# Performance work log

Hardware: AMD Instinct MI355X
Metric: run time of the kernel (lower is better)

The kernel has to match this reference:

```python
import jax, jax.numpy as jnp
import numpy as np

R = 16  # number of attention heads


def setup_inputs() -> dict:
    key = jax.random.key(0)
    ks = jax.random.split(key, 6)
    B, T, D = 2, 2048, 1024
    s = 1.0 / np.sqrt(D)
    return {
        "q": jax.random.normal(ks[0], (B, T, D), jnp.float32),
        "k": jax.random.normal(ks[1], (B, T, D), jnp.float32),
        "q_map": jax.random.normal(ks[2], (D, D), jnp.float32) * s,
        "k_map": jax.random.normal(ks[3], (D, D), jnp.float32) * s,
        "v_map": jax.random.normal(ks[4], (D, D), jnp.float32) * s,
        "output_map": jax.random.normal(ks[5], (D, D), jnp.float32) * s,
    }


def _split_heads(x, r):
    # [B, T, D] -> [B, r, T, D//r]
    B, T, D = x.shape
    return x.reshape(B, T, r, D // r).transpose(0, 2, 1, 3)


def reference(q, k, q_map, k_map, v_map, output_map):
    # v = k (the layer reuses Keys as Values)
    B, Tq, D = q.shape
    dh = D // R
    qh = _split_heads(q @ q_map, R)  # [B, r, Tq, dh]
    kh = _split_heads(k @ k_map, R)  # [B, r, Tk, dh]
    vh = _split_heads(k @ v_map, R)  # [B, r, Tk, dh]
    scale = 1.0 / jnp.sqrt(jnp.asarray(dh, qh.dtype))
    scores = jnp.einsum('brqd,brkd->brqk', qh, kh) * scale
    weights = jax.nn.softmax(scores, axis=-1)  # dropout=0 / inference -> identity
    out = jnp.einsum('brqk,brkd->brqd', weights, vh)  # [B, r, Tq, dh]
    merged = out.transpose(0, 2, 1, 3).reshape(B, Tq, D)
    return merged @ output_map
```

## Files before the change

kernel.cpp:

```cpp
#include <hip/hip_runtime.h>
#include <hip/hip_bf16.h>


typedef unsigned short u16;
typedef __attribute__((ext_vector_type(8))) short short8;
typedef __attribute__((ext_vector_type(4))) float f32x4;

__device__ __forceinline__ u16 f2bf(float f) {
  __hip_bfloat16 h = __float2bfloat16(f);
  return reinterpret_cast<u16&>(h);
}

__device__ __forceinline__ void gl_lds16(const u16* g, u16* l) {
  __builtin_amdgcn_global_load_lds(
      (const __attribute__((address_space(1))) void*)g,
      (__attribute__((address_space(3))) void*)l, 16, 0, 0);
}

template <int ROWS>
__device__ __forceinline__ void stage_tile(const u16* __restrict__ g, int gs,
                                           u16* lds, int wave, int lane) {
  const int lr8 = lane >> 3;
  const int gc = ((lane & 7) ^ lr8) * 8;
#pragma unroll
  for (int w = 0; w < ROWS / 32; ++w) {
    int t = w * 4 + wave;
    gl_lds16(g + (size_t)(t * 8 + lr8) * gs + gc, lds + t * 512);
  }
}

__global__ __launch_bounds__(256)
void convert_qk(const float4* __restrict__ q, const float4* __restrict__ k,
                u16* __restrict__ qb, u16* __restrict__ kb) {
  int i = blockIdx.x * 256 + threadIdx.x;
  float4 qv = q[i], kv = k[i];
  ushort4 qo, ko;
  qo.x = f2bf(qv.x); qo.y = f2bf(qv.y); qo.z = f2bf(qv.z); qo.w = f2bf(qv.w);
  ko.x = f2bf(kv.x); ko.y = f2bf(kv.y); ko.z = f2bf(kv.z); ko.w = f2bf(kv.w);
  reinterpret_cast<ushort4*>(qb)[i] = qo;
  reinterpret_cast<ushort4*>(kb)[i] = ko;
}

__global__ __launch_bounds__(256)
void convert_maps(const float* __restrict__ qm, const float* __restrict__ km,
                  const float* __restrict__ vm, const float* __restrict__ om,
                  u16* __restrict__ qmT, u16* __restrict__ kmT,
                  u16* __restrict__ vmT, u16* __restrict__ omT) {
  __shared__ float t[32][33];
  const float* src; u16* dst; float scale = 1.0f;
  switch (blockIdx.z) {
    case 0:  src = qm; dst = qmT; scale = 0.125f; break;
    case 1:  src = km; dst = kmT; break;
    case 2:  src = vm; dst = vmT; break;
    default: src = om; dst = omT; break;
  }
  int nb0 = blockIdx.x * 32, kb0 = blockIdx.y * 32;
  int c = threadIdx.x & 31, rq = threadIdx.x >> 5;
#pragma unroll
  for (int j = 0; j < 4; ++j)
    t[rq * 4 + j][c] = src[(size_t)(kb0 + rq * 4 + j) * 1024 + nb0 + c];
  __syncthreads();
#pragma unroll
  for (int j = 0; j < 4; ++j) {
    int nn = rq * 4 + j;
    dst[(size_t)(nb0 + nn) * 1024 + kb0 + c] = f2bf(t[c][nn] * scale);
  }
}

template <int BN, int MODE>
__global__ __launch_bounds__(256)
void gemm128(const u16* __restrict__ A, const u16* __restrict__ Bt,
             void* __restrict__ Cv, u16* __restrict__ Vt, int K, int ldc) {
  constexpr int JF = BN / 32;
  __shared__ u16 As[2][128 * 64];
  __shared__ u16 Bs[2][BN * 64];
  const int tid = threadIdx.x;
  const int wave = tid >> 6, lane = tid & 63;
  const int lr = lane & 15, lg = lane >> 4;
  const int m0 = blockIdx.y * 128, n0 = blockIdx.x * BN;
  const int wm = (wave >> 1) * 64, wn = (wave & 1) * (BN / 2);

  f32x4 acc[4][JF] = {};
  const int kT = K >> 6;
  const u16* Ab = A + (size_t)m0 * K;
  const u16* Bb = Bt + (size_t)n0 * K;

  stage_tile<128>(Ab, K, &As[0][0], wave, lane);
  stage_tile<BN>(Bb, K, &Bs[0][0], wave, lane);
  __syncthreads();

  int cur = 0;
  for (int kt = 0; kt < kT; ++kt) {
    if (kt + 1 < kT) {
      stage_tile<128>(Ab + (kt + 1) * 64, K, &As[cur ^ 1][0], wave, lane);
      stage_tile<BN>(Bb + (kt + 1) * 64, K, &Bs[cur ^ 1][0], wave, lane);
    }
#pragma unroll
    for (int ks = 0; ks < 2; ++ks) {
      short8 af[4], bfr[JF];
#pragma unroll
      for (int i = 0; i < 4; ++i) {
        int ar = wm + i * 16 + lr;
        int ac = (ks * 4 + lg) ^ (ar & 7);
        af[i] = *reinterpret_cast<const short8*>(&As[cur][ar * 64 + ac * 8]);
      }
#pragma unroll
      for (int j = 0; j < JF; ++j) {
        int br = wn + j * 16 + lr;
        int bc = (ks * 4 + lg) ^ (br & 7);
        bfr[j] = *reinterpret_cast<const short8*>(&Bs[cur][br * 64 + bc * 8]);
      }
#pragma unroll
      for (int i = 0; i < 4; ++i)
#pragma unroll
        for (int j = 0; j < JF; ++j)
          acc[i][j] = __builtin_amdgcn_mfma_f32_16x16x32_bf16(af[i], bfr[j], acc[i][j], 0, 0, 0);
    }
    __syncthreads();
    cur ^= 1;
  }

#pragma unroll
  for (int i = 0; i < 4; ++i) {
    int row0 = m0 + wm + i * 16 + lg * 4;
#pragma unroll
    for (int j = 0; j < JF; ++j) {
      int col = n0 + wn + j * 16 + lr;
      if (MODE == 2) {
#pragma unroll
        for (int r = 0; r < 4; ++r)
          ((float*)Cv)[(size_t)(row0 + r) * ldc + col] = acc[i][j][r];
      } else if (MODE == 0) {
#pragma unroll
        for (int r = 0; r < 4; ++r)
          ((u16*)Cv)[(size_t)(row0 + r) * ldc + col] = f2bf(acc[i][j][r]);
      } else {
        if (n0 < 1024) {
#pragma unroll
          for (int r = 0; r < 4; ++r)
            ((u16*)Cv)[(size_t)(row0 + r) * ldc + col] = f2bf(acc[i][j][r]);
        } else {
          int bb = row0 >> 11, kk = row0 & 2047;
          int hd = col - 1024;
          uint2 pk;
          pk.x = (unsigned)f2bf(acc[i][j][0]) | ((unsigned)f2bf(acc[i][j][1]) << 16);
          pk.y = (unsigned)f2bf(acc[i][j][2]) | ((unsigned)f2bf(acc[i][j][3]) << 16);
          *reinterpret_cast<uint2*>(&Vt[(size_t)(bb * 1024 + hd) * 2048 + kk]) = pk;
        }
      }
    }
  }
}

__global__ __launch_bounds__(256)
void attention(const u16* __restrict__ Qp, const u16* __restrict__ Kp,
               const u16* __restrict__ Vt, u16* __restrict__ merged) {
  __shared__ u16 Ks[2][64 * 64];
  __shared__ u16 Vs[2][64 * 64];
  __shared__ u16 Ps[128 * 64];
  const int tid = threadIdx.x;
  const int wave = tid >> 6, lane = tid & 63;
  const int lr = lane & 15, lg = lane >> 4;
  const int qt = blockIdx.x, h = blockIdx.y, b = blockIdx.z;
  const int q0 = qt * 128;

  short8 qf[2][2];
#pragma unroll
  for (int qm = 0; qm < 2; ++qm) {
    const size_t qrow = (size_t)(b * 2048 + q0 + wave * 32 + qm * 16 + lr);
#pragma unroll
    for (int ks = 0; ks < 2; ++ks)
      qf[qm][ks] = *reinterpret_cast<const short8*>(
          &Qp[qrow * 1024 + h * 64 + ks * 32 + lg * 8]);
  }

  f32x4 oacc[2][4] = {};
  float ell[2] = {0.f, 0.f};

  const u16* Kg = Kp + (size_t)(b * 2048) * 1024 + h * 64;
  const u16* Vg = Vt + (size_t)(b * 1024 + h * 64) * 2048;

  stage_tile<64>(Kg, 1024, &Ks[0][0], wave, lane);
  stage_tile<64>(Vg, 2048, &Vs[0][0], wave, lane);
  __syncthreads();

  int cur = 0;
  for (int ktile = 0; ktile < 32; ++ktile) {
    if (ktile + 1 < 32) {
      const int kn = (ktile + 1) * 64;
      stage_tile<64>(Kg + (size_t)kn * 1024, 1024, &Ks[cur ^ 1][0], wave, lane);
      stage_tile<64>(Vg + kn, 2048, &Vs[cur ^ 1][0], wave, lane);
    }
#pragma unroll
    for (int qm = 0; qm < 2; ++qm) {
      const int qq = wave * 32 + qm * 16 + lr;
#pragma unroll
      for (int kf = 0; kf < 4; ++kf) {
        f32x4 z = {};
#pragma unroll
        for (int ks = 0; ks < 2; ++ks) {
          int br = kf * 16 + lr;
          int bc = (ks * 4 + lg) ^ (br & 7);
          short8 kbf = *reinterpret_cast<const short8*>(&Ks[cur][br * 64 + bc * 8]);
          z = __builtin_amdgcn_mfma_f32_16x16x32_bf16(kbf, qf[qm][ks], z, 0, 0, 0);
        }
        float p0 = __expf(z[0]), p1 = __expf(z[1]);
        float p2 = __expf(z[2]), p3 = __expf(z[3]);
        ell[qm] += (p0 + p1) + (p2 + p3);
        uint2 pk;
        pk.x = (unsigned)f2bf(p0) | ((unsigned)f2bf(p1) << 16);
        pk.y = (unsigned)f2bf(p2) | ((unsigned)f2bf(p3) << 16);
        int ch = (2 * kf + (lg >> 1)) ^ (qq & 7);
        *reinterpret_cast<uint2*>(&Ps[qq * 64 + ch * 8 + (lg & 1) * 4]) = pk;
      }
    }
    asm volatile("s_waitcnt lgkmcnt(0)" ::: "memory");
    __builtin_amdgcn_sched_barrier(0);
#pragma unroll
    for (int qm = 0; qm < 2; ++qm) {
#pragma unroll
      for (int ks = 0; ks < 2; ++ks) {
        int par = wave * 32 + qm * 16 + lr;
        int pac = (ks * 4 + lg) ^ (par & 7);
        short8 pa = *reinterpret_cast<const short8*>(&Ps[par * 64 + pac * 8]);
#pragma unroll
        for (int df = 0; df < 4; ++df) {
          int vr = df * 16 + lr;
          int vc = (ks * 4 + lg) ^ (vr & 7);
          short8 vb = *reinterpret_cast<const short8*>(&Vs[cur][vr * 64 + vc * 8]);
          oacc[qm][df] = __builtin_amdgcn_mfma_f32_16x16x32_bf16(pa, vb, oacc[qm][df], 0, 0, 0);
        }
      }
    }
    __syncthreads();
    cur ^= 1;
  }
#pragma unroll
  for (int qm = 0; qm < 2; ++qm) {
    float e = ell[qm];
    e += __shfl_xor(e, 16);
    e += __shfl_xor(e, 32);
    float inv = 1.0f / e;
    float invr[4];
#pragma unroll
    for (int r = 0; r < 4; ++r) invr[r] = __shfl(inv, lg * 4 + r);
    const size_t rowbase = (size_t)(b * 2048 + q0 + wave * 32 + qm * 16 + lg * 4);
#pragma unroll
    for (int df = 0; df < 4; ++df)
#pragma unroll
      for (int r = 0; r < 4; ++r)
        merged[(rowbase + r) * 1024 + h * 64 + df * 16 + lr] =
            f2bf(oacc[qm][df][r] * invr[r]);
  }
}

extern "C" void kernel_launch(void* const* d_in, const int* in_sizes, int n_in,
                              void* d_out, int out_size, void* d_ws, size_t ws_size,
                              hipStream_t stream) {
  const float* q  = (const float*)d_in[0];
  const float* k  = (const float*)d_in[1];
  const float* qm = (const float*)d_in[2];
  const float* km = (const float*)d_in[3];
  const float* vm = (const float*)d_in[4];
  const float* om = (const float*)d_in[5];
  float* out = (float*)d_out;

  char* w = (char*)d_ws;
  const size_t MB = 1024 * 1024;
  u16* qb  = (u16*)(w + 0 * MB);
  u16* kb  = (u16*)(w + 8 * MB);
  u16* qmT = (u16*)(w + 16 * MB);
  u16* kmT = (u16*)(w + 18 * MB);
  u16* vmT = (u16*)(w + 20 * MB);
  u16* omT = (u16*)(w + 22 * MB);
  u16* Qp  = (u16*)(w + 24 * MB);
  u16* Kp  = (u16*)(w + 32 * MB);
  u16* Vt  = (u16*)(w + 48 * MB);
  u16* merged = qb;

  convert_qk<<<4096, 256, 0, stream>>>((const float4*)q, (const float4*)k, qb, kb);
  convert_maps<<<dim3(32, 32, 4), 256, 0, stream>>>(qm, km, vm, om, qmT, kmT, vmT, omT);
  gemm128<64, 0><<<dim3(16, 32), 256, 0, stream>>>(qb, qmT, Qp, nullptr, 1024, 1024);
  gemm128<128, 1><<<dim3(16, 32), 256, 0, stream>>>(kb, kmT, Kp, Vt, 1024, 1024);
  attention<<<dim3(16, 16, 2), 256, 0, stream>>>(Qp, Kp, Vt, merged);
  gemm128<64, 2><<<dim3(16, 32), 256, 0, stream>>>(merged, omT, out, nullptr, 1024, 1024);
}
```

Measured before the change: 219.1 us.

## Merge QKV projection GEMMs and pass attention probabilities through registers

The Q projection and the K/V projection become one launch, gemm_qkv, which treats the contiguous transposed Q, K and V maps as one 3072-column B matrix and picks the A input and output layout from the block column. The attention kernel now gives each wave a single 16-row query fragment, so blocks hold 64 queries and the grid doubles. Softmax probabilities move from the score-MFMA output layout into the PV-MFMA operand layout with cross-lane shuffles instead of a round trip through shared memory. This removes a kernel launch, the P shared-memory buffer and its wait, and should raise occupancy. The cost is extra shuffle instructions, and K/V tiles are now reloaded for half as many queries per block.

Measured after the change: 242.9 us. +10.9%, slower.

```diff
diff --git a/kernel.cpp b/kernel.cpp
--- a/kernel.cpp
+++ b/kernel.cpp
@@ -67,37 +67,115 @@
   }
 }
 
-template <int BN, int MODE>
-__global__ __launch_bounds__(256)
-void gemm128(const u16* __restrict__ A, const u16* __restrict__ Bt,
-             void* __restrict__ Cv, u16* __restrict__ Vt, int K, int ldc) {
-  constexpr int JF = BN / 32;
+__global__ __launch_bounds__(256)
+void gemm_qkv(const u16* __restrict__ qb, const u16* __restrict__ kb,
+              const u16* __restrict__ Bt, u16* __restrict__ Qp,
+              u16* __restrict__ Kp, u16* __restrict__ Vt) {
   __shared__ u16 As[2][128 * 64];
-  __shared__ u16 Bs[2][BN * 64];
+  __shared__ u16 Bs[2][128 * 64];
   const int tid = threadIdx.x;
   const int wave = tid >> 6, lane = tid & 63;
   const int lr = lane & 15, lg = lane >> 4;
-  const int m0 = blockIdx.y * 128, n0 = blockIdx.x * BN;
-  const int wm = (wave >> 1) * 64, wn = (wave & 1) * (BN / 2);
-
-  f32x4 acc[4][JF] = {};
+  const int xx = blockIdx.x;
+  const int m0 = blockIdx.y * 128, n0 = xx * 128;
+  const int wm = (wave >> 1) * 64, wn = (wave & 1) * 64;
+  const u16* A = (xx < 8) ? qb : kb;
+
+  f32x4 acc[4][4] = {};
+  const int K = 1024;
+  const u16* Ab = A + (size_t)m0 * K;
+  const u16* Bb = Bt + (size_t)n0 * K;
+
+  stage_tile<128>(Ab, K, &As[0][0], wave, lane);
+  stage_tile<128>(Bb, K, &Bs[0][0], wave, lane);
+  __syncthreads();
+
+  int cur = 0;
+  for (int kt = 0; kt < 16; ++kt) {
+    if (kt + 1 < 16) {
+      stage_tile<128>(Ab + (kt + 1) * 64, K, &As[cur ^ 1][0], wave, lane);
+      stage_tile<128>(Bb + (kt + 1) * 64, K, &Bs[cur ^ 1][0], wave, lane);
+    }
+#pragma unroll
+    for (int ks = 0; ks < 2; ++ks) {
+      short8 af[4], bfr[4];
+#pragma unroll
+      for (int i = 0; i < 4; ++i) {
+        int ar = wm + i * 16 + lr;
+        int ac = (ks * 4 + lg) ^ (ar & 7);
+        af[i] = *reinterpret_cast<const short8*>(&As[cur][ar * 64 + ac * 8]);
+      }
+#pragma unroll
+      for (int j = 0; j < 4; ++j) {
+        int br = wn + j * 16 + lr;
+        int bc = (ks * 4 + lg) ^ (br & 7);
+        bfr[j] = *reinterpret_cast<const short8*>(&Bs[cur][br * 64 + bc * 8]);
+      }
+#pragma unroll
+      for (int i = 0; i < 4; ++i)
+#pragma unroll
+        for (int j = 0; j < 4; ++j)
+          acc[i][j] = __builtin_amdgcn_mfma_f32_16x16x32_bf16(af[i], bfr[j], acc[i][j], 0, 0, 0);
+    }
+    __syncthreads();
+    cur ^= 1;
+  }
+
+#pragma unroll
+  for (int i = 0; i < 4; ++i) {
+    int row0 = m0 + wm + i * 16 + lg * 4;
+#pragma unroll
+    for (int j = 0; j < 4; ++j) {
+      int col = n0 + wn + j * 16 + lr;
+      if (xx < 8) {
+#pragma unroll
+        for (int r = 0; r < 4; ++r)
+          Qp[(size_t)(row0 + r) * 1024 + col] = f2bf(acc[i][j][r]);
+      } else if (xx < 16) {
+#pragma unroll
+        for (int r = 0; r < 4; ++r)
+          Kp[(size_t)(row0 + r) * 1024 + (col - 1024)] = f2bf(acc[i][j][r]);
+      } else {
+        int bb = row0 >> 11, kk = row0 & 2047;
+        int hd = col - 2048;
+        uint2 pk;
+        pk.x = (unsigned)f2bf(acc[i][j][0]) | ((unsigned)f2bf(acc[i][j][1]) << 16);
+        pk.y = (unsigned)f2bf(acc[i][j][2]) | ((unsigned)f2bf(acc[i][j][3]) << 16);
+        *reinterpret_cast<uint2*>(&Vt[(size_t)(bb * 1024 + hd) * 2048 + kk]) = pk;
+      }
+    }
+  }
+}
+
+__global__ __launch_bounds__(256)
+void gemm_out(const u16* __restrict__ A, const u16* __restrict__ Bt,
+              float* __restrict__ C, int K, int ldc) {
+  __shared__ u16 As[2][128 * 64];
+  __shared__ u16 Bs[2][64 * 64];
+  const int tid = threadIdx.x;
+  const int wave = tid >> 6, lane = tid & 63;
+  const int lr = lane & 15, lg = lane >> 4;
+  const int m0 = blockIdx.y * 128, n0 = blockIdx.x * 64;
+  const int wm = (wave >> 1) * 64, wn = (wave & 1) * 32;
+
+  f32x4 acc[4][2] = {};
   const int kT = K >> 6;
   const u16* Ab = A + (size_t)m0 * K;
   const u16* Bb = Bt + (size_t)n0 * K;
 
   stage_tile<128>(Ab, K, &As[0][0], wave, lane);
-  stage_tile<BN>(Bb, K, &Bs[0][0], wave, lane);
+  stage_tile<64>(Bb, K, &Bs[0][0], wave, lane);
   __syncthreads();
 
   int cur = 0;
   for (int kt = 0; kt < kT; ++kt) {
     if (kt + 1 < kT) {
       stage_tile<128>(Ab + (kt + 1) * 64, K, &As[cur ^ 1][0], wave, lane);
-      stage_tile<BN>(Bb + (kt + 1) * 64, K, &Bs[cur ^ 1][0], wave, lane);
+      stage_tile<64>(Bb + (kt + 1) * 64, K, &Bs[cur ^ 1][0], wave, lane);
     }
 #pragma unroll
     for (int ks = 0; ks < 2; ++ks) {
-      short8 af[4], bfr[JF];
+      short8 af[4], bfr[2];
 #pragma unroll
       for (int i = 0; i < 4; ++i) {
         int ar = wm + i * 16 + lr;
@@ -105,7 +183,7 @@
         af[i] = *reinterpret_cast<const short8*>(&As[cur][ar * 64 + ac * 8]);
       }
 #pragma unroll
-      for (int j = 0; j < JF; ++j) {
+      for (int j = 0; j < 2; ++j) {
         int br = wn + j * 16 + lr;
         int bc = (ks * 4 + lg) ^ (br & 7);
         bfr[j] = *reinterpret_cast<const short8*>(&Bs[cur][br * 64 + bc * 8]);
@@ -113,41 +191,21 @@
 #pragma unroll
       for (int i = 0; i < 4; ++i)
 #pragma unroll
-        for (int j = 0; j < JF; ++j)
+        for (int j = 0; j < 2; ++j)
           acc[i][j] = __builtin_amdgcn_mfma_f32_16x16x32_bf16(af[i], bfr[j], acc[i][j], 0, 0, 0);
     }
     __syncthreads();
     cur ^= 1;
   }
-
 #pragma unroll
   for (int i = 0; i < 4; ++i) {
     int row0 = m0 + wm + i * 16 + lg * 4;
 #pragma unroll
-    for (int j = 0; j < JF; ++j) {
+    for (int j = 0; j < 2; ++j) {
       int col = n0 + wn + j * 16 + lr;
-      if (MODE == 2) {
-#pragma unroll
-        for (int r = 0; r < 4; ++r)
-          ((float*)Cv)[(size_t)(row0 + r) * ldc + col] = acc[i][j][r];
-      } else if (MODE == 0) {
-#pragma unroll
-        for (int r = 0; r < 4; ++r)
-          ((u16*)Cv)[(size_t)(row0 + r) * ldc + col] = f2bf(acc[i][j][r]);
-      } else {
-        if (n0 < 1024) {
-#pragma unroll
-          for (int r = 0; r < 4; ++r)
-            ((u16*)Cv)[(size_t)(row0 + r) * ldc + col] = f2bf(acc[i][j][r]);
-        } else {
-          int bb = row0 >> 11, kk = row0 & 2047;
-          int hd = col - 1024;
-          uint2 pk;
-          pk.x = (unsigned)f2bf(acc[i][j][0]) | ((unsigned)f2bf(acc[i][j][1]) << 16);
-          pk.y = (unsigned)f2bf(acc[i][j][2]) | ((unsigned)f2bf(acc[i][j][3]) << 16);
-          *reinterpret_cast<uint2*>(&Vt[(size_t)(bb * 1024 + hd) * 2048 + kk]) = pk;
-        }
-      }
+#pragma unroll
+      for (int r = 0; r < 4; ++r)
+        C[(size_t)(row0 + r) * ldc + col] = acc[i][j][r];
     }
   }
 }
@@ -157,25 +215,19 @@
                const u16* __restrict__ Vt, u16* __restrict__ merged) {
   __shared__ u16 Ks[2][64 * 64];
   __shared__ u16 Vs[2][64 * 64];
-  __shared__ u16 Ps[128 * 64];
   const int tid = threadIdx.x;
   const int wave = tid >> 6, lane = tid & 63;
   const int lr = lane & 15, lg = lane >> 4;
   const int qt = blockIdx.x, h = blockIdx.y, b = blockIdx.z;
-  const int q0 = qt * 128;
-
-  short8 qf[2][2];
-#pragma unroll
-  for (int qm = 0; qm < 2; ++qm) {
-    const size_t qrow = (size_t)(b * 2048 + q0 + wave * 32 + qm * 16 + lr);
-#pragma unroll
-    for (int ks = 0; ks < 2; ++ks)
-      qf[qm][ks] = *reinterpret_cast<const short8*>(
-          &Qp[qrow * 1024 + h * 64 + ks * 32 + lg * 8]);
-  }
-
-  f32x4 oacc[2][4] = {};
-  float ell[2] = {0.f, 0.f};
+  const int q0 = qt * 64;
+
+  short8 qf[2];
+  const size_t qrow = (size_t)(b * 2048 + q0 + wave * 16 + lr);
+  qf[0] = *reinterpret_cast<const short8*>(&Qp[qrow * 1024 + h * 64 + lg * 8]);
+  qf[1] = *reinterpret_cast<const short8*>(&Qp[qrow * 1024 + h * 64 + 32 + lg * 8]);
+
+  f32x4 oacc[4] = {};
+  float ell = 0.f;
 
   const u16* Kg = Kp + (size_t)(b * 2048) * 1024 + h * 64;
   const u16* Vg = Vt + (size_t)(b * 1024 + h * 64) * 2048;
@@ -191,67 +243,66 @@
       stage_tile<64>(Kg + (size_t)kn * 1024, 1024, &Ks[cur ^ 1][0], wave, lane);
       stage_tile<64>(Vg + kn, 2048, &Vs[cur ^ 1][0], wave, lane);
     }
-#pragma unroll
-    for (int qm = 0; qm < 2; ++qm) {
-      const int qq = wave * 32 + qm * 16 + lr;
-#pragma unroll
-      for (int kf = 0; kf < 4; ++kf) {
-        f32x4 z = {};
-#pragma unroll
-        for (int ks = 0; ks < 2; ++ks) {
-          int br = kf * 16 + lr;
-          int bc = (ks * 4 + lg) ^ (br & 7);
-          short8 kbf = *reinterpret_cast<const short8*>(&Ks[cur][br * 64 + bc * 8]);
-          z = __builtin_amdgcn_mfma_f32_16x16x32_bf16(kbf, qf[qm][ks], z, 0, 0, 0);
-        }
-        float p0 = __expf(z[0]), p1 = __expf(z[1]);
-        float p2 = __expf(z[2]), p3 = __expf(z[3]);
-        ell[qm] += (p0 + p1) + (p2 + p3);
-        uint2 pk;
-        pk.x = (unsigned)f2bf(p0) | ((unsigned)f2bf(p1) << 16);
-        pk.y = (unsigned)f2bf(p2) | ((unsigned)f2bf(p3) << 16);
-        int ch = (2 * kf + (lg >> 1)) ^ (qq & 7);
-        *reinterpret_cast<uint2*>(&Ps[qq * 64 + ch * 8 + (lg & 1) * 4]) = pk;
-      }
-    }
-    asm volatile("s_waitcnt lgkmcnt(0)" ::: "memory");
-    __builtin_amdgcn_sched_barrier(0);
-#pragma unroll
-    for (int qm = 0; qm < 2; ++qm) {
+    unsigned W[4][2];
+#pragma unroll
+    for (int kf = 0; kf < 4; ++kf) {
+      f32x4 z = {};
 #pragma unroll
       for (int ks = 0; ks < 2; ++ks) {
-        int par = wave * 32 + qm * 16 + lr;
-        int pac = (ks * 4 + lg) ^ (par & 7);
-        short8 pa = *reinterpret_cast<const short8*>(&Ps[par * 64 + pac * 8]);
-#pragma unroll
-        for (int df = 0; df < 4; ++df) {
-          int vr = df * 16 + lr;
-          int vc = (ks * 4 + lg) ^ (vr & 7);
-          short8 vb = *reinterpret_cast<const short8*>(&Vs[cur][vr * 64 + vc * 8]);
-          oacc[qm][df] = __builtin_amdgcn_mfma_f32_16x16x32_bf16(pa, vb, oacc[qm][df], 0, 0, 0);
-        }
+        int br = kf * 16 + lr;
+        int bc = (ks * 4 + lg) ^ (br & 7);
+        short8 kbf = *reinterpret_cast<const short8*>(&Ks[cur][br * 64 + bc * 8]);
+        z = __builtin_amdgcn_mfma_f32_16x16x32_bf16(kbf, qf[ks], z, 0, 0, 0);
+      }
+      float p0 = __expf(z[0]), p1 = __expf(z[1]);
+      float p2 = __expf(z[2]), p3 = __expf(z[3]);
+      ell += (p0 + p1) + (p2 + p3);
+      W[kf][0] = (unsigned)f2bf(p0) | ((unsigned)f2bf(p1) << 16);
+      W[kf][1] = (unsigned)f2bf(p2) | ((unsigned)f2bf(p3) << 16);
+    }
+    const int src01 = lr + ((lg & 1) << 5);
+    const int src23 = src01 + 16;
+    const bool hiq = lg >= 2;
+#pragma unroll
+    for (int ks = 0; ks < 2; ++ks) {
+      unsigned lo0 = (unsigned)__shfl((int)W[ks * 2][0],     src01);
+      unsigned hi0 = (unsigned)__shfl((int)W[ks * 2 + 1][0], src01);
+      unsigned lo1 = (unsigned)__shfl((int)W[ks * 2][1],     src01);
+      unsigned hi1 = (unsigned)__shfl((int)W[ks * 2 + 1][1], src01);
+      unsigned lo2 = (unsigned)__shfl((int)W[ks * 2][0],     src23);
+      unsigned hi2 = (unsigned)__shfl((int)W[ks * 2 + 1][0], src23);
+      unsigned lo3 = (unsigned)__shfl((int)W[ks * 2][1],     src23);
+      unsigned hi3 = (unsigned)__shfl((int)W[ks * 2 + 1][1], src23);
+      union { uint4 u; short8 s; } pu;
+      pu.u.x = hiq ? hi0 : lo0;
+      pu.u.y = hiq ? hi1 : lo1;
+      pu.u.z = hiq ? hi2 : lo2;
+      pu.u.w = hiq ? hi3 : lo3;
+#pragma unroll
+      for (int df = 0; df < 4; ++df) {
+        int vr = df * 16 + lr;
+        int vc = (ks * 4 + lg) ^ (vr & 7);
+        short8 vb = *reinterpret_cast<const short8*>(&Vs[cur][vr * 64 + vc * 8]);
+        oacc[df] = __builtin_amdgcn_mfma_f32_16x16x32_bf16(pu.s, vb, oacc[df], 0, 0, 0);
       }
     }
     __syncthreads();
     cur ^= 1;
   }
-#pragma unroll
-  for (int qm = 0; qm < 2; ++qm) {
-    float e = ell[qm];
-    e += __shfl_xor(e, 16);
-    e += __shfl_xor(e, 32);
-    float inv = 1.0f / e;
-    float invr[4];
-#pragma unroll
-    for (int r = 0; r < 4; ++r) invr[r] = __shfl(inv, lg * 4 + r);
-    const size_t rowbase = (size_t)(b * 2048 + q0 + wave * 32 + qm * 16 + lg * 4);
-#pragma unroll
-    for (int df = 0; df < 4; ++df)
-#pragma unroll
-      for (int r = 0; r < 4; ++r)
-        merged[(rowbase + r) * 1024 + h * 64 + df * 16 + lr] =
-            f2bf(oacc[qm][df][r] * invr[r]);
-  }
+  float e = ell;
+  e += __shfl_xor(e, 16);
+  e += __shfl_xor(e, 32);
+  float inv = 1.0f / e;
+  float invr[4];
+#pragma unroll
+  for (int r = 0; r < 4; ++r) invr[r] = __shfl(inv, lg * 4 + r);
+  const size_t rowbase = (size_t)(b * 2048 + q0 + wave * 16 + lg * 4);
+#pragma unroll
+  for (int df = 0; df < 4; ++df)
+#pragma unroll
+    for (int r = 0; r < 4; ++r)
+      merged[(rowbase + r) * 1024 + h * 64 + df * 16 + lr] =
+          f2bf(oacc[df][r] * invr[r]);
 }
 
 extern "C" void kernel_launch(void* const* d_in, const int* in_sizes, int n_in,
@@ -280,8 +331,7 @@
 
   convert_qk<<<4096, 256, 0, stream>>>((const float4*)q, (const float4*)k, qb, kb);
   convert_maps<<<dim3(32, 32, 4), 256, 0, stream>>>(qm, km, vm, om, qmT, kmT, vmT, omT);
-  gemm128<64, 0><<<dim3(16, 32), 256, 0, stream>>>(qb, qmT, Qp, nullptr, 1024, 1024);
-  gemm128<128, 1><<<dim3(16, 32), 256, 0, stream>>>(kb, kmT, Kp, Vt, 1024, 1024);
-  attention<<<dim3(16, 16, 2), 256, 0, stream>>>(Qp, Kp, Vt, merged);
-  gemm128<64, 2><<<dim3(16, 32), 256, 0, stream>>>(merged, omT, out, nullptr, 1024, 1024);
-}
+  gemm_qkv<<<dim3(24, 32), 256, 0, stream>>>(qb, kb, qmT, Qp, Kp, Vt);
+  attention<<<dim3(32, 16, 2), 256, 0, stream>>>(Qp, Kp, Vt, merged);
+  gemm_out<<<dim3(16, 32), 256, 0, stream>>>(merged, omT, out, 1024, 1024);
+}
```
